# Optimization experiments

Measured on AMD Instinct MI355X. Metric: run time of the kernel, lower is better.

## Reference

```python
import jax, jax.numpy as jnp
import numpy as np

TEMPERATURE = 0.1
B, T, D = 8, 1024, 1024
NEG_INF = -1e30

def setup_inputs() -> dict:
    key = jax.random.key(0)
    k1, k2, k3 = jax.random.split(key, 3)
    features = jax.random.normal(k1, (B, T, D), dtype=jnp.float32)
    masks = jax.random.bernoulli(k2, 0.05, (B, 1, T, T)).astype(jnp.float32)
    input_coords_length = jax.random.randint(k3, (B,), T // 2, T - 1)  # int32
    return {"features": features, "masks": masks, "input_coords_length": input_coords_length}


def _sup_con_loss(feat, mask, L):
    # feat: [T, D], mask: [T, T] float, L: scalar int valid length (slice [:L, :L])
    Tn = feat.shape[0]
    dt = feat.dtype
    vr = jnp.arange(Tn) < L                              # valid rows/cols [T]
    valid2d = (vr[:, None] & vr[None, :]).astype(dt)     # [T, T]
    dot = jnp.matmul(feat, feat.T) / TEMPERATURE         # [T, T]
    dot = jnp.where(vr[None, :], dot, NEG_INF)           # exclude padded cols from max
    logits = dot - jax.lax.stop_gradient(jnp.max(dot, axis=-1, keepdims=True))
    logits_mask = (1.0 - jnp.eye(Tn, dtype=dt)) * valid2d  # off-diagonal, in-slice
    exp_logits = jnp.exp(logits) * logits_mask
    m = mask * valid2d
    # negative_mask = 1-mask; entries < 1 zeroed (binary mask -> indicator of mask==0)
    neg = 1.0 - m
    neg = jnp.where(neg < 1.0, 0.0, neg) * valid2d
    # positive_mask = mask with entries > 0 set to 1
    pos = jnp.where(m > 0, 1.0, m)
    neg_denom = jnp.sum(exp_logits * neg, axis=-1, keepdims=True)
    pos_denom = jax.lax.stop_gradient(jnp.sum(exp_logits * pos, axis=-1, keepdims=True))
    log_prob = logits - jnp.log(neg_denom + pos_denom + 1e-6)
    m2 = m * logits_mask
    mean_log_prob_pos = (m2 * log_prob).sum(-1) / (m2.sum(-1) + 1e-6)  # [T]
    # mean over the L valid rows only (matches .mean() on the sliced tensor)
    return -jnp.sum(jnp.where(vr, mean_log_prob_pos, 0.0)) / L.astype(dt)


def _is_valid(mask, L):
    # valid sample iff sliced mask differs from eye(L) with [0,0]=0
    Tn = mask.shape[0]
    vr = jnp.arange(Tn) < L
    valid2d = (vr[:, None] & vr[None, :]).astype(mask.dtype)
    sanity = jnp.eye(Tn, dtype=mask.dtype).at[0, 0].set(0.0) * valid2d
    return jnp.any((mask * valid2d) != sanity)


def reference(features, masks, input_coords_length):
    L = input_coords_length + 1                      # [B]
    mask0 = masks[:, 0]                              # [B, T, T] (num_layers asserted == 1)
    losses = jax.vmap(_sup_con_loss)(features, mask0, L)   # [B]
    valid = jax.vmap(_is_valid)(mask0, L)                  # [B] bool
    vbs = jnp.maximum(jnp.sum(valid.astype(features.dtype)), 1.0)
    return jnp.sum(losses) / vbs
```

## Files before the change

kernel.cpp:

```cpp
#include <hip/hip_runtime.h>
#include <hip/hip_bf16.h>
#include <stdint.h>

#define T_DIM 1024
#define B_DIM 8

typedef __attribute__((ext_vector_type(8))) short short8;
typedef __attribute__((ext_vector_type(4))) float f32x4;

__device__ inline void gll16(const void* g, void* l) {
  __builtin_amdgcn_global_load_lds((__attribute__((address_space(1))) void*)g,
                                   (__attribute__((address_space(3))) void*)l,
                                   16, 0, 0);
}

__global__ __launch_bounds__(256) void convert_kernel(const float* __restrict__ F,
                                                      __hip_bfloat16* __restrict__ Fb) {
  const int t = blockIdx.x * 256 + threadIdx.x;
  const float4 v = ((const float4*)F)[t];
  union { __hip_bfloat16 h[4]; uint64_t u; } p;
  p.h[0] = __float2bfloat16(v.x);
  p.h[1] = __float2bfloat16(v.y);
  p.h[2] = __float2bfloat16(v.z);
  p.h[3] = __float2bfloat16(v.w);
  ((uint64_t*)Fb)[t] = p.u;
}

__global__ __launch_bounds__(512) void fused_kernel(const __hip_bfloat16* __restrict__ Fb,
                                                    const float* __restrict__ M,
                                                    const int* __restrict__ icl,
                                                    float* __restrict__ part) {
  const int b  = blockIdx.z;
  const int rt = blockIdx.y;
  const int ct = blockIdx.x;
  const int L  = icl[b] + 1;
  if (rt * 128 >= L || ct * 128 >= L) return;

  __shared__ char smem[65536];
  __hip_bfloat16* As = (__hip_bfloat16*)smem;
  __hip_bfloat16* Bs = (__hip_bfloat16*)(smem + 32768);
  float* rp = (float*)smem;
  float* rp_m = rp;
  float* rp_d = rp + 512;
  float* rp_s = rp + 1024;
  float* rp_c = rp + 1536;
  float* rp_b = rp + 2048;

  const __hip_bfloat16* F = Fb + ((size_t)b << 20);
  const int tid  = threadIdx.x;
  const int lane = tid & 63;
  const int wave = tid >> 6;
  const int wrow = (wave >> 2) * 64;
  const int wcol = (wave & 3) * 32;
  const int row0 = rt * 128;
  const int col0 = ct * 128;
  const bool diag = (rt == ct);

  const int fr = lane & 15;
  const int q  = lane >> 4;
  const int sl8 = (q ^ ((fr >> 1) & 3)) * 8;

  const int srow = tid >> 2;
  const int sgk  = (((tid & 3) ^ ((tid >> 3) & 3)) * 8);

  f32x4 acc[4][2];
#pragma unroll
  for (int i = 0; i < 4; i++)
#pragma unroll
    for (int j = 0; j < 2; j++) acc[i][j] = (f32x4){0.f, 0.f, 0.f, 0.f};

  for (int k0 = 0; k0 < T_DIM; k0 += 128) {
    __syncthreads();
#pragma unroll
    for (int p = 0; p < 4; p++)
      gll16(F + (size_t)(row0 + srow) * T_DIM + k0 + p * 32 + sgk,
            As + p * 4096 + tid * 8);
    if (!diag) {
#pragma unroll
      for (int p = 0; p < 4; p++)
        gll16(F + (size_t)(col0 + srow) * T_DIM + k0 + p * 32 + sgk,
              Bs + p * 4096 + tid * 8);
    }
    __syncthreads();
#pragma unroll
    for (int kk = 0; kk < 4; kk++) {
      const __hip_bfloat16* Ab = As + kk * 4096;
      const __hip_bfloat16* Bb = diag ? Ab : (Bs + kk * 4096);
      short8 af[4], bfr[2];
#pragma unroll
      for (int t = 0; t < 4; t++)
        af[t] = *(const short8*)(Ab + (wrow + t * 16 + fr) * 32 + sl8);
#pragma unroll
      for (int j = 0; j < 2; j++)
        bfr[j] = *(const short8*)(Bb + (wcol + j * 16 + fr) * 32 + sl8);
#pragma unroll
      for (int ti = 0; ti < 4; ti++)
#pragma unroll
        for (int tj = 0; tj < 2; tj++)
          acc[ti][tj] = __builtin_amdgcn_mfma_f32_16x16x32_bf16(af[ti], bfr[tj], acc[ti][tj], 0, 0, 0);
    }
  }
  __syncthreads();

  const float* Mb = M + ((size_t)b << 20);
  const int gc0 = col0 + wcol + fr;
  const int gc1 = gc0 + 16;
#pragma unroll
  for (int ti = 0; ti < 4; ti++) {
    float mk0[4], mk1[4];
#pragma unroll
    for (int r = 0; r < 4; r++) {
      const int grow = row0 + wrow + ti * 16 + q * 4 + r;
      mk0[r] = (gc0 < L) ? Mb[(size_t)grow * T_DIM + gc0] : 0.f;
      mk1[r] = (gc1 < L) ? Mb[(size_t)grow * T_DIM + gc1] : 0.f;
    }
#pragma unroll
    for (int r = 0; r < 4; r++) {
      const int lrow = wrow + ti * 16 + q * 4 + r;
      const int grow = row0 + lrow;
      const float s0 = (gc0 < L) ? acc[ti][0][r] * 10.0f : -1e30f;
      const float s1 = (gc1 < L) ? acc[ti][1][r] * 10.0f : -1e30f;
      float m = fmaxf(s0, s1);
#pragma unroll
      for (int d = 1; d < 16; d <<= 1) m = fmaxf(m, __shfl_xor(m, d, 64));
      float den = 0.f, msum = 0.f, cnt = 0.f, badf = 0.f;
      if (gc0 < L) {
        if (gc0 != grow) { den += __expf(s0 - m); msum += mk0[r] * s0; cnt += mk0[r]; }
        const float sane = (gc0 == grow && grow != 0) ? 1.f : 0.f;
        badf = fmaxf(badf, (mk0[r] != sane) ? 1.f : 0.f);
      }
      if (gc1 < L) {
        if (gc1 != grow) { den += __expf(s1 - m); msum += mk1[r] * s1; cnt += mk1[r]; }
        const float sane = (gc1 == grow && grow != 0) ? 1.f : 0.f;
        badf = fmaxf(badf, (mk1[r] != sane) ? 1.f : 0.f);
      }
#pragma unroll
      for (int d = 1; d < 16; d <<= 1) {
        den  += __shfl_xor(den, d, 64);
        msum += __shfl_xor(msum, d, 64);
        cnt  += __shfl_xor(cnt, d, 64);
        badf  = fmaxf(badf, __shfl_xor(badf, d, 64));
      }
      if (fr == 0) {
        const int slot = wave & 3;
        rp_m[lrow * 4 + slot] = m;   rp_d[lrow * 4 + slot] = den;
        rp_s[lrow * 4 + slot] = msum; rp_c[lrow * 4 + slot] = cnt;
        rp_b[lrow * 4 + slot] = badf;
      }
    }
  }
  __syncthreads();

  if (tid < 128) {
    float m = -1e30f;
#pragma unroll
    for (int s = 0; s < 4; s++) m = fmaxf(m, rp_m[tid * 4 + s]);
    float den = 0.f, msum = 0.f, cnt = 0.f, badf = 0.f;
#pragma unroll
    for (int s = 0; s < 4; s++) {
      den  += rp_d[tid * 4 + s] * __expf(rp_m[tid * 4 + s] - m);
      msum += rp_s[tid * 4 + s];
      cnt  += rp_c[tid * 4 + s];
      badf  = fmaxf(badf, rp_b[tid * 4 + s]);
    }
    float* p = part + ((((size_t)b * 1024 + row0 + tid) * 8) + ct) * 5;
    p[0] = m; p[1] = den; p[2] = msum; p[3] = cnt; p[4] = badf;
  }
}

__global__ __launch_bounds__(256) void reduce_kernel(const float* __restrict__ part,
                                                     const int* __restrict__ icl,
                                                     float* __restrict__ blk_sum,
                                                     int* __restrict__ blk_bad) {
  const int blk = blockIdx.x;
  const int row = blk * 256 + threadIdx.x;
  const int b = row >> 10;
  const int i = row & 1023;
  const int L = icl[b] + 1;
  float rv = 0.f;
  int bad = 0;
  if (i < L) {
    const float* p = part + (size_t)row * 40;
    const int ns = (L + 127) >> 7;
    float m = -1e30f;
    for (int s = 0; s < ns; s++) m = fmaxf(m, p[s * 5 + 0]);
    float den = 0.f, msum = 0.f, cnt = 0.f, badf = 0.f;
    for (int s = 0; s < ns; s++) {
      den  += p[s * 5 + 1] * __expf(p[s * 5 + 0] - m);
      msum += p[s * 5 + 2];
      cnt  += p[s * 5 + 3];
      badf  = fmaxf(badf, p[s * 5 + 4]);
    }
    const float A = msum - cnt * m;
    const float mlpp = (A - cnt * __logf(den + 1e-6f)) / (cnt + 1e-6f);
    rv = -mlpp / (float)L;
    bad = badf > 0.f ? 1 : 0;
  }
  const int tid  = threadIdx.x;
  const int lane = tid & 63;
  const int wave = tid >> 6;
  for (int o = 32; o > 0; o >>= 1) rv += __shfl_down(rv, o, 64);
  const int wbad = (__ballot(bad) != 0ull) ? 1 : 0;
  __shared__ float sred[4];
  __shared__ int bred[4];
  if (lane == 0) { sred[wave] = rv; bred[wave] = wbad; }
  __syncthreads();
  if (tid == 0) {
    blk_sum[blk] = sred[0] + sred[1] + sred[2] + sred[3];
    blk_bad[blk] = bred[0] | bred[1] | bred[2] | bred[3];
  }
}

__global__ __launch_bounds__(64) void final_kernel(const float* __restrict__ blk_sum,
                                                   const int* __restrict__ blk_bad,
                                                   float* __restrict__ out) {
  const int tid = threadIdx.x;
  float v = (tid < 32) ? blk_sum[tid] : 0.f;
  for (int o = 32; o > 0; o >>= 1) v += __shfl_down(v, o, 64);
  if (tid == 0) {
    int vcount = 0;
    for (int bb = 0; bb < B_DIM; bb++) {
      const int any = blk_bad[bb * 4] | blk_bad[bb * 4 + 1] |
                      blk_bad[bb * 4 + 2] | blk_bad[bb * 4 + 3];
      vcount += any ? 1 : 0;
    }
    out[0] = v / fmaxf((float)vcount, 1.0f);
  }
}

extern "C" void kernel_launch(void* const* d_in, const int* in_sizes, int n_in,
                              void* d_out, int out_size, void* d_ws, size_t ws_size,
                              hipStream_t stream) {
  const float* feat = (const float*)d_in[0];
  const float* mask = (const float*)d_in[1];
  const int*   icl  = (const int*)d_in[2];
  float* out = (float*)d_out;

  char* ws = (char*)d_ws;
  __hip_bfloat16* Fb = (__hip_bfloat16*)ws;
  float* part    = (float*)(ws + (16u << 20));
  float* blk_sum = (float*)(ws + (18u << 20));
  int*   blk_bad = (int*)(ws + (18u << 20) + 512);

  convert_kernel<<<dim3(8192), dim3(256), 0, stream>>>(feat, Fb);
  fused_kernel<<<dim3(8, 8, 8), dim3(512), 0, stream>>>(Fb, mask, icl, part);
  reduce_kernel<<<dim3(32), dim3(256), 0, stream>>>(part, icl, blk_sum, blk_bad);
  final_kernel<<<dim3(1), dim3(64), 0, stream>>>(blk_sum, blk_bad, out);
}
```

Before: 136.5 us.

## Double-buffer GEMM K loop and prefetch mask bits before the matmul

Splits the K loop into 16 steps of 64 with double-buffered LDS tiles, so the next tile's global-to-LDS load is issued before computing the current one, using one barrier per step instead of two. Mask values are loaded before the GEMM starts and packed into a 32-bit register bitmask, so their global latency overlaps the matmul and they take fewer registers than 32 floats. The grid is flattened with batch as the fastest index, and the launch bounds request higher occupancy. Packing to bits treats any nonzero mask entry as 1, which only matches the reference for binary masks.

```diff
diff --git a/kernel.cpp b/kernel.cpp
--- a/kernel.cpp
+++ b/kernel.cpp
@@ -26,13 +26,14 @@
   ((uint64_t*)Fb)[t] = p.u;
 }
 
-__global__ __launch_bounds__(512) void fused_kernel(const __hip_bfloat16* __restrict__ Fb,
-                                                    const float* __restrict__ M,
-                                                    const int* __restrict__ icl,
-                                                    float* __restrict__ part) {
-  const int b  = blockIdx.z;
-  const int rt = blockIdx.y;
-  const int ct = blockIdx.x;
+__global__ __launch_bounds__(512, 4) void fused_kernel(const __hip_bfloat16* __restrict__ Fb,
+                                                       const float* __restrict__ M,
+                                                       const int* __restrict__ icl,
+                                                       float* __restrict__ part) {
+  const int id = blockIdx.x;
+  const int b  = id & 7;
+  const int rt = (id >> 3) & 7;
+  const int ct = id >> 6;
   const int L  = icl[b] + 1;
   if (rt * 128 >= L || ct * 128 >= L) return;
 
@@ -63,33 +64,60 @@
   const int srow = tid >> 2;
   const int sgk  = (((tid & 3) ^ ((tid >> 3) & 3)) * 8);
 
+  const int gc0 = col0 + wcol + fr;
+  const int gc1 = gc0 + 16;
+
+  uint32_t mbits = 0;
+  {
+    const float* Mb = M + ((size_t)b << 20);
+#pragma unroll
+    for (int ti = 0; ti < 4; ti++)
+#pragma unroll
+      for (int r = 0; r < 4; r++) {
+        const int grow = row0 + wrow + ti * 16 + q * 4 + r;
+        const float* mrow = Mb + ((size_t)grow << 10);
+        const uint32_t b0 = (gc0 < L && mrow[gc0] != 0.f) ? 1u : 0u;
+        const uint32_t b1 = (gc1 < L && mrow[gc1] != 0.f) ? 1u : 0u;
+        mbits |= (b0 << (ti * 8 + r * 2)) | (b1 << (ti * 8 + r * 2 + 1));
+      }
+  }
+
   f32x4 acc[4][2];
 #pragma unroll
   for (int i = 0; i < 4; i++)
 #pragma unroll
     for (int j = 0; j < 2; j++) acc[i][j] = (f32x4){0.f, 0.f, 0.f, 0.f};
 
-  for (int k0 = 0; k0 < T_DIM; k0 += 128) {
-    __syncthreads();
-#pragma unroll
-    for (int p = 0; p < 4; p++)
-      gll16(F + (size_t)(row0 + srow) * T_DIM + k0 + p * 32 + sgk,
-            As + p * 4096 + tid * 8);
+  const size_t arow = (size_t)(row0 + srow) * T_DIM + sgk;
+  const size_t brow = (size_t)(col0 + srow) * T_DIM + sgk;
+
+  auto stage = [&](int buf, int step) {
+    const int kb = step << 6;
+#pragma unroll
+    for (int p = 0; p < 2; p++)
+      gll16(F + arow + kb + p * 32, As + buf * 8192 + p * 4096 + tid * 8);
     if (!diag) {
 #pragma unroll
-      for (int p = 0; p < 4; p++)
-        gll16(F + (size_t)(col0 + srow) * T_DIM + k0 + p * 32 + sgk,
-              Bs + p * 4096 + tid * 8);
-    }
-    __syncthreads();
-#pragma unroll
-    for (int kk = 0; kk < 4; kk++) {
-      const __hip_bfloat16* Ab = As + kk * 4096;
-      const __hip_bfloat16* Bb = diag ? Ab : (Bs + kk * 4096);
+      for (int p = 0; p < 2; p++)
+        gll16(F + brow + kb + p * 32, Bs + buf * 8192 + p * 4096 + tid * 8);
+    }
+  };
+
+  stage(0, 0);
+  __syncthreads();
+
+#pragma unroll 2
+  for (int t = 0; t < 16; t++) {
+    const int cur = t & 1;
+    if (t < 15) stage(cur ^ 1, t + 1);
+#pragma unroll
+    for (int kk = 0; kk < 2; kk++) {
+      const __hip_bfloat16* Ab = As + cur * 8192 + kk * 4096;
+      const __hip_bfloat16* Bb = diag ? Ab : (Bs + cur * 8192 + kk * 4096);
       short8 af[4], bfr[2];
 #pragma unroll
-      for (int t = 0; t < 4; t++)
-        af[t] = *(const short8*)(Ab + (wrow + t * 16 + fr) * 32 + sl8);
+      for (int tt = 0; tt < 4; tt++)
+        af[tt] = *(const short8*)(Ab + (wrow + tt * 16 + fr) * 32 + sl8);
 #pragma unroll
       for (int j = 0; j < 2; j++)
         bfr[j] = *(const short8*)(Bb + (wcol + j * 16 + fr) * 32 + sl8);
@@ -99,25 +127,17 @@
         for (int tj = 0; tj < 2; tj++)
           acc[ti][tj] = __builtin_amdgcn_mfma_f32_16x16x32_bf16(af[ti], bfr[tj], acc[ti][tj], 0, 0, 0);
     }
-  }
-  __syncthreads();
-
-  const float* Mb = M + ((size_t)b << 20);
-  const int gc0 = col0 + wcol + fr;
-  const int gc1 = gc0 + 16;
+    __syncthreads();
+  }
+
 #pragma unroll
   for (int ti = 0; ti < 4; ti++) {
-    float mk0[4], mk1[4];
-#pragma unroll
-    for (int r = 0; r < 4; r++) {
-      const int grow = row0 + wrow + ti * 16 + q * 4 + r;
-      mk0[r] = (gc0 < L) ? Mb[(size_t)grow * T_DIM + gc0] : 0.f;
-      mk1[r] = (gc1 < L) ? Mb[(size_t)grow * T_DIM + gc1] : 0.f;
-    }
 #pragma unroll
     for (int r = 0; r < 4; r++) {
       const int lrow = wrow + ti * 16 + q * 4 + r;
       const int grow = row0 + lrow;
+      const float mk0 = (float)((mbits >> (ti * 8 + r * 2)) & 1u);
+      const float mk1 = (float)((mbits >> (ti * 8 + r * 2 + 1)) & 1u);
       const float s0 = (gc0 < L) ? acc[ti][0][r] * 10.0f : -1e30f;
       const float s1 = (gc1 < L) ? acc[ti][1][r] * 10.0f : -1e30f;
       float m = fmaxf(s0, s1);
@@ -125,14 +145,14 @@
       for (int d = 1; d < 16; d <<= 1) m = fmaxf(m, __shfl_xor(m, d, 64));
       float den = 0.f, msum = 0.f, cnt = 0.f, badf = 0.f;
       if (gc0 < L) {
-        if (gc0 != grow) { den += __expf(s0 - m); msum += mk0[r] * s0; cnt += mk0[r]; }
+        if (gc0 != grow) { den += __expf(s0 - m); msum += mk0 * s0; cnt += mk0; }
         const float sane = (gc0 == grow && grow != 0) ? 1.f : 0.f;
-        badf = fmaxf(badf, (mk0[r] != sane) ? 1.f : 0.f);
+        badf = fmaxf(badf, (mk0 != sane) ? 1.f : 0.f);
       }
       if (gc1 < L) {
-        if (gc1 != grow) { den += __expf(s1 - m); msum += mk1[r] * s1; cnt += mk1[r]; }
+        if (gc1 != grow) { den += __expf(s1 - m); msum += mk1 * s1; cnt += mk1; }
         const float sane = (gc1 == grow && grow != 0) ? 1.f : 0.f;
-        badf = fmaxf(badf, (mk1[r] != sane) ? 1.f : 0.f);
+        badf = fmaxf(badf, (mk1 != sane) ? 1.f : 0.f);
       }
 #pragma unroll
       for (int d = 1; d < 16; d <<= 1) {
@@ -243,7 +263,7 @@
   int*   blk_bad = (int*)(ws + (18u << 20) + 512);
 
   convert_kernel<<<dim3(8192), dim3(256), 0, stream>>>(feat, Fb);
-  fused_kernel<<<dim3(8, 8, 8), dim3(512), 0, stream>>>(Fb, mask, icl, part);
+  fused_kernel<<<dim3(512), dim3(512), 0, stream>>>(Fb, mask, icl, part);
   reduce_kernel<<<dim3(32), dim3(256), 0, stream>>>(part, icl, blk_sum, blk_bad);
   final_kernel<<<dim3(1), dim3(64), 0, stream>>>(blk_sum, blk_bad, out);
 }
```

New measurement: 139.5 us. +2.2%, slower.
